# Kernel optimization log

Measured on AMD Instinct MI355X. Metric: run time of the kernel, lower is better.

The kernel has to match this reference:

```python
import jax, jax.numpy as jnp
import numpy as np
import math

B, CIN, COUT, NSC, H, W = 4, 3, 64, 3, 192, 192
HID = 64  # attention hidden channels


def setup_inputs() -> dict:
    key = jax.random.key(0)
    ks = jax.random.split(key, 10)
    pi = math.pi
    return {
        "x": jax.random.normal(ks[0], (B, CIN, H, W), jnp.float32),
        "freq": jax.random.uniform(ks[1], (NSC, COUT, CIN), jnp.float32) * pi,
        "theta": jax.random.uniform(ks[2], (NSC, COUT, CIN), jnp.float32) * pi,
        "sigma": jax.random.uniform(ks[3], (NSC, COUT, CIN), jnp.float32) * pi,
        "f0": jnp.ones((NSC, COUT, CIN), jnp.float32),
        "theta0": jnp.ones((NSC, COUT, CIN), jnp.float32),
        "attn_w1": jax.random.normal(ks[4], (HID, CIN), jnp.float32) / np.sqrt(CIN).astype(np.float32),
        "attn_b1": jnp.zeros((HID,), jnp.float32),
        "attn_w2": jax.random.normal(ks[5], (COUT * NSC, HID), jnp.float32) / np.sqrt(HID).astype(np.float32),
        "attn_b2": jnp.zeros((COUT * NSC,), jnp.float32),
        "bn_w": jnp.ones((COUT * NSC,), jnp.float32),
        "bn_b": jnp.zeros((COUT * NSC,), jnp.float32),
        "mixing_param": jax.random.uniform(ks[6], (1,), jnp.float32),
        "conv_w": jax.random.normal(ks[7], (COUT, CIN, 3, 3), jnp.float32) * 0.1,
        "freq_band_select": jax.random.uniform(ks[8], (COUT, CIN, 2), jnp.float32),
    }


def _forward(x, freq, theta, sigma, f0, theta0, attn_w1, attn_b1, attn_w2,
             attn_b2, bn_w, bn_b, mixing_param, conv_w, freq_band_select):
    b, cin, h, w = x.shape
    # torch.fft.fftshift default dim=None shifts ALL axes (incl. batch/channel)
    Xs = jnp.fft.fftshift(jnp.fft.fft2(x))  # [B,Cin,H,W] complex64

    # ---- multi-scale log-Gabor filter bank g[S,O,I,H,W] ----
    yy, xx = jnp.meshgrid(jnp.linspace(-1.0, 1.0, h), jnp.linspace(-1.0, 1.0, w), indexing="ij")
    r = jnp.sqrt(xx * xx + yy * yy + 1e-6)
    phi = jnp.arctan2(yy, xx)
    f0e = f0[..., None, None]
    sg = sigma[..., None, None]
    th = theta[..., None, None]
    th0 = theta0[..., None, None]
    fr = freq[..., None, None]
    log_gabor = jnp.exp(-(jnp.log(r) - jnp.log(f0e)) ** 2 / (2.0 * jnp.log(sg / f0e) ** 2))
    angular = jnp.exp(-(phi - th) ** 2 / (2.0 * th0 ** 2))
    g = log_gabor * angular * jnp.cos(fr * r) / (2.0 * math.pi * sg ** 2)  # [S,O,I,H,W]

    # ---- frequency attention: 1x1 conv -> ReLU -> 1x1 conv -> BN(train) -> softmax ----
    mag = jnp.abs(Xs)
    h1 = jax.nn.relu(jnp.einsum("oi,bihw->bohw", attn_w1, mag) + attn_b1[None, :, None, None])
    h2 = jnp.einsum("oi,bihw->bohw", attn_w2, h1) + attn_b2[None, :, None, None]
    mu = h2.mean(axis=(0, 2, 3))
    var = h2.var(axis=(0, 2, 3))  # biased, as torch BN training mode
    h2 = (h2 - mu[None, :, None, None]) * jax.lax.rsqrt(var + 1e-5)[None, :, None, None]
    h2 = h2 * bn_w[None, :, None, None] + bn_b[None, :, None, None]
    attn = jax.nn.softmax(h2, axis=1).reshape(b, NSC, COUT, h, w)  # view as [B,S,O,H,W]

    # ---- attention-weighted complex sum over (scale, out, in), then batch ----
    # attended_output(b) = sum_{s,o,i} attn[b,s,o]*g[s,o,i]*Xs[b,i]; torch then
    # sums over Cin and, via the [B,O,B,I,H,W] broadcast + sum(dims 2,3), over batch.
    Wr = jnp.einsum("bsohw,soihw->bihw", attn, g)  # real attention*filter weights
    A_tot = (Wr * Xs).sum(axis=(0, 1))             # [H,W] complex

    # ---- per-(out,in) frequency band mask (same index range on both axes) ----
    idx = jnp.floor((freq_band_select + 1.0) * 0.5 * h).astype(jnp.int32)  # [O,I,2]
    hr = jnp.arange(h)
    c = (hr[None, None, :] >= idx[..., 0:1]) & (hr[None, None, :] < idx[..., 1:2])  # [O,I,H]
    mask = (c[:, :, :, None] & c[:, :, None, :]).astype(jnp.float32)  # [O,I,H,W]
    Msum = mask.sum(axis=1)  # [O,H,W] (sum over Cin)

    # torch builds r[b0,o,b2,i,h,w]=A[b2]*M[o,i], ifftshift(all axes), ifft2,
    # real, sum over (b2,i). Rolls on summed axes commute with the sums, so this
    # equals ifftshift over (b0,o,h,w) of Q[b0,o]=A_tot*Msum[o] (const in b0).
    Q = jnp.broadcast_to((A_tot[None] * Msum.astype(Xs.dtype))[None], (b, COUT, h, w))
    xf = jnp.fft.ifft2(jnp.fft.ifftshift(Q)).real  # [B,O,H,W]

    xs = jax.lax.conv_general_dilated(
        x, conv_w, window_strides=(1, 1), padding=((1, 1), (1, 1)),
        dimension_numbers=("NCHW", "OIHW", "NCHW"))
    return mixing_param * xf + (1.0 - mixing_param) * xs


def reference(x, freq, theta, sigma, f0, theta0, attn_w1, attn_b1, attn_w2,
              attn_b2, bn_w, bn_b, mixing_param, conv_w, freq_band_select):
    return _forward(x, freq, theta, sigma, f0, theta0, attn_w1, attn_b1,
                    attn_w2, attn_b2, bn_w, bn_b, mixing_param, conv_w,
                    freq_band_select)
```

## Files before the change

kernel.cpp:

```cpp
#include <hip/hip_runtime.h>
#include <math.h>

#define NPIX  36864
#define PI2   6.28318530717958647692f

#define TW_OFF    0
#define PCA_OFF   1536
#define PCB_OFF   10752
#define W1F4_OFF  15360
#define W2B_OFF   16384
#define BN_OFF    65536
#define IDX_OFF   67072
#define M2_OFF    68608
#define T1_OFF    85248
#define XS_OFF    3624192
#define AH_OFF    7163136
#define XF_OFF    7458048
#define E2B_OFF   15846656
#define WS_FUSED  7458048
#define WS_SPLIT  16895232

#define PH_BYTES  14155776
#define E2C_OFF   14155776
#define OUT_MIN_ELEMS 9437184

typedef __attribute__((ext_vector_type(8))) short short8;
typedef __attribute__((ext_vector_type(4))) float floatx4;

__device__ __forceinline__ void bf16split(float v, unsigned short& hi, unsigned short& lo) {
    unsigned ub = __builtin_bit_cast(unsigned, v);
    hi = (unsigned short)(ub >> 16);
    float vh = __builtin_bit_cast(float, ub & 0xFFFF0000u);
    lo = (unsigned short)(__builtin_bit_cast(unsigned, v - vh) >> 16);
}

__global__ void k_pre(const float* freq, const float* theta, const float* sigma,
                      const float* f0, const float* theta0, const float* fbs,
                      const float* w1, const float* b1v, const float* w2,
                      char* ws, char* outw, int split) {
    float2* tw   = (float2*)(ws + TW_OFF);
    float4* pcA  = (float4*)(ws + PCA_OFF);
    float2* pcB  = (float2*)(ws + PCB_OFF);
    float4* w1f4 = (float4*)(ws + W1F4_OFF);
    unsigned short* w2b = (unsigned short*)(ws + W2B_OFF);
    int* idx = (int*)(ws + IDX_OFF);
    int gtid = blockIdx.x * blockDim.x + threadIdx.x;
    int gsz  = gridDim.x * blockDim.x;
    for (int n = gtid; n < 192; n += gsz) {
        float th = PI2 * (float)n / 192.0f;
        tw[n] = make_float2(cosf(th), sinf(th));
    }
    for (int t = gtid; t < 576; t += gsz) {
        int s = t / 192, rem = t % 192, o = rem / 3, i = rem % 3;
        float fr = freq[t], th = theta[t], sg = sigma[t], f0v = f0[t], th0 = theta0[t];
        float lg  = logf(sg / f0v);
        float a1  = -1.0f / (2.0f * lg * lg);
        float lf0 = logf(f0v);
        float a2  = -1.0f / (2.0f * th0 * th0);
        float lsc = -logf(PI2 * sg * sg);
        int pidx = (s*3 + i)*64 + o;
        pcA[pidx] = make_float4(a1, lf0, a2, th);
        pcB[pidx] = make_float2(fr, lsc);
    }
    for (int t = gtid; t < 64; t += gsz)
        w1f4[t] = make_float4(w1[t*3+0], w1[t*3+1], w1[t*3+2], b1v[t]);
    for (int u = gtid; u < 24576; u += gsz) {
        int j = u & 7;
        int l = (u >> 3) & 63;
        int hsel = (u >> 9) & 1;
        int rest = u >> 10;
        int kc = rest & 1;
        int t = rest >> 1;
        int k = kc*32 + (l>>4)*8 + j;
        int c = t*16 + (l & 15);
        float wv = w2[c*64 + k];
        unsigned short hi, lo;
        bf16split(wv, hi, lo);
        w2b[u] = hsel ? lo : hi;
    }
    for (int t = gtid; t < 192; t += gsz) {
        int lo = (int)floorf((fbs[t*2+0] + 1.0f) * 0.5f * 192.0f) - 96;
        int hi = (int)floorf((fbs[t*2+1] + 1.0f) * 0.5f * 192.0f) - 96;
        lo = max(0, min(96, lo));
        hi = max(0, min(96, hi));
        if (hi < lo) hi = lo;
        idx[t*2+0] = lo; idx[t*2+1] = hi;
    }
    if (split) {
        unsigned short* e2b = (unsigned short*)(ws + E2B_OFF);
        for (int u = gtid; u < 147456; u += gsz) {
            int j = u & 7;
            int l = (u >> 3) & 63;
            int half = (u >> 9) & 1;
            int rest = u >> 10;
            int kc = rest % 12, t = rest / 12;
            int k = kc*32 + ((l >> 4) << 3) + j;
            int w = k >> 1, comp = k & 1;
            int n = t*16 + (l & 15);
            int ang = (w * n) % 192;
            float th = PI2 * (float)ang / 192.0f;
            float v = comp ? sinf(th) : cosf(th);
            unsigned short hi, lo;
            bf16split(v, hi, lo);
            e2b[u] = half ? lo : hi;
        }
        unsigned short* e1 = (unsigned short*)(ws + T1_OFF);
        for (int u = gtid; u < 147456; u += gsz) {
            int j = u & 7;
            int l = (u >> 3) & 63;
            int half = (u >> 9) & 1;
            int rest = u >> 10;
            int kc = rest % 6;
            int comp = (rest / 6) & 1;
            int yt = rest / 12;
            int y = yt*16 + (l & 15);
            int h = kc*32 + ((l >> 4) << 3) + j;
            int ang = (h * y) % 192;
            float th = PI2 * (float)ang / 192.0f;
            float v = comp ? -sinf(th) : cosf(th);
            unsigned short hi, lo;
            bf16split(v, hi, lo);
            e1[u] = half ? lo : hi;
        }
        unsigned short* e2c = (unsigned short*)(outw + E2C_OFF);
        for (int u = gtid; u < 73728; u += gsz) {
            int j = u & 7;
            int l = (u >> 3) & 63;
            int half = (u >> 9) & 1;
            int rest = u >> 10;
            int kc = rest % 6, t = rest / 6;
            int k = kc*32 + ((l >> 4) << 3) + j;
            int w = k >> 1, comp = k & 1;
            int n = t*16 + (l & 15);
            int ang = (w * n) % 192;
            float th = PI2 * (float)ang / 192.0f;
            float v = comp ? sinf(th) : cosf(th);
            unsigned short hi, lo;
            bf16split(v, hi, lo);
            e2c[u] = half ? lo : hi;
        }
    }
}

__global__ __launch_bounds__(256) void k_dftm(const float* x, char* ws) {
    __shared__ __align__(16) float2 Ar[16][194];
    const unsigned short* e1  = (const unsigned short*)(ws + T1_OFF);
    const unsigned short* e2b = (const unsigned short*)(ws + E2B_OFF);
    float2* Xs = (float2*)(ws + XS_OFF);
    int tid = threadIdx.x;
    int bi = blockIdx.x / 12;
    int yt = blockIdx.x % 12;
    int y0 = yt * 16;
    int wave = tid >> 6, lane = tid & 63;
    int ml = lane & 15, qd = lane >> 4;
    const float* xp = x + bi * NPIX;
    union AB { short8 v; unsigned short u[8]; };
    floatx4 s1re[3], s1im[3];
#pragma unroll
    for (int tt = 0; tt < 3; tt++) {
        s1re[tt] = (floatx4){0.f,0.f,0.f,0.f};
        s1im[tt] = (floatx4){0.f,0.f,0.f,0.f};
    }
#pragma unroll 1
    for (int kc = 0; kc < 6; kc++) {
        const unsigned short* ac = e1 + (((((yt*2 + 0)*6 + kc)*2) << 9) + (lane << 3));
        const unsigned short* as = e1 + (((((yt*2 + 1)*6 + kc)*2) << 9) + (lane << 3));
        short8 ach = *(const short8*)ac;
        short8 acl = *(const short8*)(ac + 512);
        short8 ash = *(const short8*)as;
        short8 asl = *(const short8*)(as + 512);
#pragma unroll
        for (int tt = 0; tt < 3; tt++) {
            int nt = wave*3 + tt;
            AB bh8, bl8;
#pragma unroll
            for (int j = 0; j < 8; j++) {
                int h = kc*32 + qd*8 + j;
                float xv = xp[h*192 + nt*16 + ml];
                bf16split(xv, bh8.u[j], bl8.u[j]);
            }
            floatx4 r = s1re[tt];
            r = __builtin_amdgcn_mfma_f32_16x16x32_bf16(ach, bh8.v, r, 0, 0, 0);
            r = __builtin_amdgcn_mfma_f32_16x16x32_bf16(acl, bh8.v, r, 0, 0, 0);
            r = __builtin_amdgcn_mfma_f32_16x16x32_bf16(ach, bl8.v, r, 0, 0, 0);
            s1re[tt] = r;
            floatx4 q = s1im[tt];
            q = __builtin_amdgcn_mfma_f32_16x16x32_bf16(ash, bh8.v, q, 0, 0, 0);
            q = __builtin_amdgcn_mfma_f32_16x16x32_bf16(asl, bh8.v, q, 0, 0, 0);
            q = __builtin_amdgcn_mfma_f32_16x16x32_bf16(ash, bl8.v, q, 0, 0, 0);
            s1im[tt] = q;
        }
    }
#pragma unroll
    for (int tt = 0; tt < 3; tt++) {
        int w = (wave*3 + tt)*16 + ml;
#pragma unroll
        for (int r = 0; r < 4; r++)
            Ar[qd*4 + r][w] = make_float2(s1re[tt][r], s1im[tt][r]);
    }
    __syncthreads();
    floatx4 accre[3], accim[3];
#pragma unroll
    for (int tt = 0; tt < 3; tt++) {
        accre[tt] = (floatx4){0.f,0.f,0.f,0.f};
        accim[tt] = (floatx4){0.f,0.f,0.f,0.f};
    }
#pragma unroll 1
    for (int kc = 0; kc < 12; kc++) {
        int wb = kc*16 + qd*4;
        float4 p01 = *(const float4*)&Ar[ml][wb];
        float4 p23 = *(const float4*)&Ar[ml][wb + 2];
        float av[8]  = {p01.x, p01.y, p01.z, p01.w, p23.x, p23.y, p23.z, p23.w};
        float apv[8] = {p01.y, -p01.x, p01.w, -p01.z, p23.y, -p23.x, p23.w, -p23.z};
        AB ah, al, aph, apl;
#pragma unroll
        for (int j = 0; j < 8; j++) {
            bf16split(av[j],  ah.u[j],  al.u[j]);
            bf16split(apv[j], aph.u[j], apl.u[j]);
        }
#pragma unroll
        for (int tt = 0; tt < 3; tt++) {
            int t = wave*3 + tt;
            const unsigned short* bp = e2b + (((t*12 + kc)*2) << 9) + (lane << 3);
            short8 bh = *(const short8*)bp;
            short8 bl = *(const short8*)(bp + 512);
            floatx4 r = accre[tt];
            r = __builtin_amdgcn_mfma_f32_16x16x32_bf16(ah.v,  bh, r, 0, 0, 0);
            r = __builtin_amdgcn_mfma_f32_16x16x32_bf16(al.v,  bh, r, 0, 0, 0);
            r = __builtin_amdgcn_mfma_f32_16x16x32_bf16(ah.v,  bl, r, 0, 0, 0);
            accre[tt] = r;
            floatx4 q = accim[tt];
            q = __builtin_amdgcn_mfma_f32_16x16x32_bf16(aph.v, bh, q, 0, 0, 0);
            q = __builtin_amdgcn_mfma_f32_16x16x32_bf16(apl.v, bh, q, 0, 0, 0);
            q = __builtin_amdgcn_mfma_f32_16x16x32_bf16(aph.v, bl, q, 0, 0, 0);
            accim[tt] = q;
        }
    }
    int b = bi / 3, i = bi % 3;
    int bs = (b + 2) & 3;
    int is = (i + 1) % 3;
    float2* Xp = Xs + (bs*3 + is)*NPIX;
#pragma unroll
    for (int tt = 0; tt < 3; tt++) {
        int kx = (wave*3 + tt)*16 + ml;
        int ks = kx + 96; if (ks >= 192) ks -= 192;
#pragma unroll
        for (int r = 0; r < 4; r++) {
            int y = y0 + qd*4 + r;
            int ys = y + 96; if (ys >= 192) ys -= 192;
            Xp[ys*192 + ks] = make_float2(accre[tt][r], accim[tt][r]);
        }
    }
}

__global__ __launch_bounds__(192) void k_dft1(const float* x, char* ws) {
    __shared__ float2 twsh[192];
    const float2* tw = (const float2*)(ws + TW_OFF);
    float2* t1 = (float2*)(ws + T1_OFF);
    int tid = threadIdx.x;
    twsh[tid] = tw[tid];
    __syncthreads();
    int bi = blockIdx.x;
    int y0 = blockIdx.y * 4;
    int w  = tid;
    const float* xp = x + bi * NPIX;
    float2 acc[4];
#pragma unroll
    for (int d = 0; d < 4; d++) acc[d] = make_float2(0.f, 0.f);
    for (int h = 0; h < 192; h++) {
        float xv = xp[h*192 + w];
        int m = (h * y0) % 192;
#pragma unroll
        for (int d = 0; d < 4; d++) {
            float2 e = twsh[m];
            acc[d].x += xv * e.x;
            acc[d].y -= xv * e.y;
            m += h; if (m >= 192) m -= 192;
        }
    }
    float2* op = t1 + bi * NPIX;
#pragma unroll
    for (int d = 0; d < 4; d++) op[(y0 + d)*192 + w] = acc[d];
}

__global__ __launch_bounds__(192) void k_dft2(char* ws) {
    __shared__ float2 twsh[192];
    __shared__ float2 row[192];
    const float2* tw = (const float2*)(ws + TW_OFF);
    const float2* t1a = (const float2*)(ws + T1_OFF);
    float2* Xs = (float2*)(ws + XS_OFF);
    int tid = threadIdx.x;
    int bi = blockIdx.x, y = blockIdx.y;
    twsh[tid] = tw[tid];
    row[tid] = t1a[bi*NPIX + y*192 + tid];
    __syncthreads();
    int kx = tid;
    float2 st = twsh[kx];
    float2 acc = make_float2(0.f, 0.f);
#pragma unroll 1
    for (int w0 = 0; w0 < 192; w0 += 32) {
        float2 e = twsh[(w0 * kx) % 192];
#pragma unroll
        for (int w = 0; w < 32; w++) {
            float2 t = row[w0 + w];
            acc.x += t.x*e.x + t.y*e.y;
            acc.y += t.y*e.x - t.x*e.y;
            float ex = e.x*st.x - e.y*st.y;
            e.y = e.x*st.y + e.y*st.x;
            e.x = ex;
        }
    }
    int b = bi / 3, i = bi % 3;
    int bs = (b + 2) & 3;
    int is = (i + 1) % 3;
    int ys = y + 96;  if (ys >= 192) ys -= 192;
    int ks = kx + 96; if (ks >= 192) ks -= 192;
    Xs[(bs*3 + is)*NPIX + ys*192 + ks] = acc;
}

__global__ __launch_bounds__(256) void k_stats(char* ws) {
    __shared__ float magL[192];
    __shared__ float4 w1L[64];
    __shared__ float m1L[64];
    __shared__ __align__(16) unsigned short fragH[512*8];
    __shared__ __align__(16) unsigned short fragL[512*8];
    const float2* Xs = (const float2*)(ws + XS_OFF);
    float* M2 = (float*)(ws + M2_OFF);
    int tid = threadIdx.x;
    int wave = tid >> 6, lane = tid & 63;
    if (tid < 64) { w1L[tid] = ((const float4*)(ws + W1F4_OFF))[tid]; m1L[tid] = 0.f; }
    __syncthreads();
    int cch = wave*16 + (lane & 15);
    float4 wf = w1L[cch];
    float msum = 0.f;
    floatx4 acc[4];
#pragma unroll
    for (int nb = 0; nb < 4; nb++) acc[nb] = (floatx4){0.f, 0.f, 0.f, 0.f};
    union AB { short8 v; unsigned short u[8]; };
#pragma unroll 1
    for (int it = 0; it < 2; it++) {
        int tile = blockIdx.x * 2 + it;
        int S0 = tile * 64;
        int b = S0 / NPIX;
        int p0 = S0 - b*NPIX;
        if (tid < 192) {
            int i = tid >> 6, s = tid & 63;
            float2 v = Xs[(b*3 + i)*NPIX + p0 + s];
            magL[s*3 + i] = sqrtf(v.x*v.x + v.y*v.y);
        }
        __syncthreads();
#pragma unroll
        for (int kc = 0; kc < 2; kc++) {
            AB h8, l8;
#pragma unroll
            for (int j = 0; j < 8; j++) {
                int s = kc*32 + (lane>>4)*8 + j;
                float mg0 = magL[s*3], mg1 = magL[s*3+1], mg2 = magL[s*3+2];
                float hv = fmaxf(wf.w + wf.x*mg0 + wf.y*mg1 + wf.z*mg2, 0.f);
                msum += hv;
                bf16split(hv, h8.u[j], l8.u[j]);
            }
            int z = (kc*4 + wave)*64 + lane;
            *(short8*)&fragH[z*8] = h8.v;
            *(short8*)&fragL[z*8] = l8.v;
        }
        __syncthreads();
        short8 Ah0 = *(const short8*)&fragH[((0*4+wave)*64 + lane)*8];
        short8 Ah1 = *(const short8*)&fragH[((1*4+wave)*64 + lane)*8];
        short8 Al0 = *(const short8*)&fragL[((0*4+wave)*64 + lane)*8];
        short8 Al1 = *(const short8*)&fragL[((1*4+wave)*64 + lane)*8];
#pragma unroll
        for (int nb = 0; nb < 4; nb++) {
            short8 Bh0 = *(const short8*)&fragH[((0*4+nb)*64 + lane)*8];
            short8 Bh1 = *(const short8*)&fragH[((1*4+nb)*64 + lane)*8];
            short8 Bl0 = *(const short8*)&fragL[((0*4+nb)*64 + lane)*8];
            short8 Bl1 = *(const short8*)&fragL[((1*4+nb)*64 + lane)*8];
            floatx4 a = acc[nb];
            a = __builtin_amdgcn_mfma_f32_16x16x32_bf16(Ah0, Bh0, a, 0, 0, 0);
            a = __builtin_amdgcn_mfma_f32_16x16x32_bf16(Al0, Bh0, a, 0, 0, 0);
            a = __builtin_amdgcn_mfma_f32_16x16x32_bf16(Ah0, Bl0, a, 0, 0, 0);
            a = __builtin_amdgcn_mfma_f32_16x16x32_bf16(Ah1, Bh1, a, 0, 0, 0);
            a = __builtin_amdgcn_mfma_f32_16x16x32_bf16(Al1, Bh1, a, 0, 0, 0);
            a = __builtin_amdgcn_mfma_f32_16x16x32_bf16(Ah1, Bl1, a, 0, 0, 0);
            acc[nb] = a;
        }
        __syncthreads();
    }
#pragma unroll
    for (int nb = 0; nb < 4; nb++)
#pragma unroll
        for (int r = 0; r < 4; r++) {
            int row = wave*16 + (lane>>4)*4 + r;
            int col = nb*16 + (lane & 15);
            atomicAdd(&M2[row*64 + col], acc[nb][r]);
        }
    atomicAdd(&m1L[cch], msum);
    __syncthreads();
    if (tid < 64) atomicAdd(&M2[4096 + tid], m1L[tid]);
}

__global__ __launch_bounds__(64) void k_bn(const float* w2, const float* bnw,
                                           const float* bnb, char* ws) {
    const float* M2 = (const float*)(ws + M2_OFF);
    const float* m1 = M2 + 4096;
    float* bnsc = (float*)(ws + BN_OFF);
    float* bnsh = bnsc + 192;
    int c = blockIdx.x;
    int jj = threadIdx.x;
    const float* row = w2 + c*64;
    float rj = row[jj];
    float inner = 0.f;
    const float* m2r = M2 + jj*64;
    for (int k = 0; k < 64; k++) inner += row[k] * m2r[k];
    float qpart = rj * inner;
    float dpart = rj * m1[jj];
#pragma unroll
    for (int sh = 32; sh >= 1; sh >>= 1) {
        qpart += __shfl_xor(qpart, sh);
        dpart += __shfl_xor(dpart, sh);
    }
    if (jj == 0) {
        const float invN = 1.0f / 147456.0f;
        float d = dpart * invN;
        float qv = qpart * invN;
        float var = qv - d*d;
        float rstd = rsqrtf(var + 1e-5f);
        float scale = bnw[c] * rstd;
        bnsc[c] = scale;
        bnsh[c] = bnb[c] - d * scale;
    }
}

__global__ __launch_bounds__(256) void k_attn(char* ws) {
    __shared__ __align__(16) float4 pcAL[576];
    __shared__ float2 pcBL[576];
    __shared__ float4 w1L[64];
    const float2* Xs = (const float2*)(ws + XS_OFF);
    const float* bnA = (const float*)(ws + BN_OFF);
    const char* W2G = (const char*)(ws + W2B_OFF);
    float2* Ah = (float2*)(ws + AH_OFF);
    int tid = threadIdx.x;
    {
        const float4* pcA4 = (const float4*)(ws + PCA_OFF);
        const float2* pcB2 = (const float2*)(ws + PCB_OFF);
        for (int u = tid; u < 576; u += 256) {
            pcAL[u] = pcA4[u];
            pcBL[u] = pcB2[u];
        }
        if (tid < 64) w1L[tid] = ((const float4*)(ws + W1F4_OFF))[tid];
    }
    __syncthreads();
    int wave = tid >> 6, lane = tid & 63;
    int cl = lane & 15, q = lane >> 4;
    int g = blockIdx.x * 4 + wave;
    int pix0 = g * 4;

    union AB { short8 v; unsigned short u[8]; };
    int pb = pix0 + (cl >> 2), bb = cl & 3;
    float2 q0 = Xs[(bb*3+0)*NPIX + pb];
    float2 q1 = Xs[(bb*3+1)*NPIX + pb];
    float2 q2 = Xs[(bb*3+2)*NPIX + pb];
    float mg0 = sqrtf(q0.x*q0.x + q0.y*q0.y);
    float mg1 = sqrtf(q1.x*q1.x + q1.y*q1.y);
    float mg2 = sqrtf(q2.x*q2.x + q2.y*q2.y);
    AB ah[2], al[2];
#pragma unroll
    for (int kc = 0; kc < 2; kc++)
#pragma unroll
        for (int j = 0; j < 8; j++) {
            int k = kc*32 + q*8 + j;
            float4 wf = w1L[k];
            float hv = fmaxf(wf.w + wf.x*mg0 + wf.y*mg1 + wf.z*mg2, 0.f);
            bf16split(hv, ah[kc].u[j], al[kc].u[j]);
        }
    int pixE = pix0 + q;
    int hh = pixE / 192, ww = pixE - hh*192;
    float yy = -1.0f + (float)hh * (2.0f/191.0f);
    float xx = -1.0f + (float)ww * (2.0f/191.0f);
    float rr = sqrtf(xx*xx + yy*yy + 1e-6f);
    float lr = __logf(rr);
    float phi = atan2f(yy, xx);
    float sm0 = 0.f, sm1 = 0.f, sm2 = 0.f, sm3 = 0.f;
    float Wr[4][3];
#pragma unroll
    for (int r = 0; r < 4; r++) { Wr[r][0] = 0.f; Wr[r][1] = 0.f; Wr[r][2] = 0.f; }
#pragma unroll 2
    for (int t = 0; t < 12; t++) {
        floatx4 a = {0.f, 0.f, 0.f, 0.f};
#pragma unroll
        for (int kc = 0; kc < 2; kc++) {
            int ob = (((t*2 + kc)*2)*64 + lane)*16;
            short8 bh = *(const short8*)(W2G + ob);
            short8 bl = *(const short8*)(W2G + ob + 1024);
            a = __builtin_amdgcn_mfma_f32_16x16x32_bf16(ah[kc].v, bh, a, 0, 0, 0);
            a = __builtin_amdgcn_mfma_f32_16x16x32_bf16(al[kc].v, bh, a, 0, 0, 0);
            a = __builtin_amdgcn_mfma_f32_16x16x32_bf16(ah[kc].v, bl, a, 0, 0, 0);
        }
        int c = t*16 + cl;
        float sc_ = bnA[c], sh_ = bnA[192 + c];
        float e0 = __expf(a[0]*sc_ + sh_);
        float e1 = __expf(a[1]*sc_ + sh_);
        float e2 = __expf(a[2]*sc_ + sh_);
        float e3 = __expf(a[3]*sc_ + sh_);
        sm0 += e0; sm1 += e1; sm2 += e2; sm3 += e3;
        int sB = c >> 6, o = c & 63;
#pragma unroll
        for (int i = 0; i < 3; i++) {
            int pidx = (sB*3 + i)*64 + o;
            float4 pa = pcAL[pidx];
            float2 pbv = pcBL[pidx];
            float dl = lr - pa.y, dp = phi - pa.w;
            float gv = __expf(pa.x*dl*dl + pa.z*dp*dp + pbv.y) * __cosf(pbv.x*rr);
            Wr[0][i] += e0*gv; Wr[1][i] += e1*gv;
            Wr[2][i] += e2*gv; Wr[3][i] += e3*gv;
        }
    }
#pragma unroll
    for (int sh = 1; sh < 16; sh <<= 1) {
        sm0 += __shfl_xor(sm0, sh); sm1 += __shfl_xor(sm1, sh);
        sm2 += __shfl_xor(sm2, sh); sm3 += __shfl_xor(sm3, sh);
    }
    float inv0 = 1.0f/sm0, inv1 = 1.0f/sm1, inv2 = 1.0f/sm2, inv3 = 1.0f/sm3;
    float are = 0.f, aim = 0.f;
#pragma unroll
    for (int i = 0; i < 3; i++) {
        float2 x0 = Xs[(0*3+i)*NPIX + pixE];
        float2 x1 = Xs[(1*3+i)*NPIX + pixE];
        float2 x2 = Xs[(2*3+i)*NPIX + pixE];
        float2 x3 = Xs[(3*3+i)*NPIX + pixE];
        float w0v = Wr[0][i]*inv0, w1v = Wr[1][i]*inv1;
        float w2v = Wr[2][i]*inv2, w3v = Wr[3][i]*inv3;
        are += w0v*x0.x + w1v*x1.x + w2v*x2.x + w3v*x3.x;
        aim += w0v*x0.y + w1v*x1.y + w2v*x2.y + w3v*x3.y;
    }
#pragma unroll
    for (int sh = 1; sh < 16; sh <<= 1) {
        are += __shfl_xor(are, sh);
        aim += __shfl_xor(aim, sh);
    }
    if (cl == 0) {
        int hs = hh + 96; if (hs >= 192) hs -= 192;
        int wsx = ww + 96; if (wsx >= 192) wsx -= 192;
        Ah[hs*192 + wsx] = make_float2(are, aim);
    }
}

__global__ __launch_bounds__(64) void k_phpre(char* ws, char* outw) {
    __shared__ float2 AhL[96];
    const float2* tw  = (const float2*)(ws + TW_OFF);
    const float2* Ahp = (const float2*)(ws + AH_OFF);
    float2* Ph = (float2*)outw;
    int tid = threadIdx.x;
    int y = blockIdx.y * 64 + tid;
    int w = blockIdx.x;
    for (int u = tid; u < 96; u += 64) AhL[u] = Ahp[u*192 + w];
    __syncthreads();
    float2 step = tw[y];
    float ex = 1.f, ey = 0.f;
    float ax = 0.f, ay = 0.f;
    for (int h = 0; h < 96; h++) {
        float2 a = AhL[h];
        ax += a.x*ex - a.y*ey;
        ay += a.x*ey + a.y*ex;
        Ph[(h*96 + w)*192 + y] = make_float2(ax, ay);
        float t = ex*step.x - ey*step.y;
        ey = ex*step.y + ey*step.x;
        ex = t;
    }
}

__global__ __launch_bounds__(256) void k_ifftm(char* ws, char* outw) {
    __shared__ __align__(16) unsigned short AhiL[16*200];
    __shared__ __align__(16) unsigned short AloL[16*200];
    __shared__ int iL[3], iH[3];
    const float2* Ph = (const float2*)outw;
    const unsigned short* e2c = (const unsigned short*)(outw + E2C_OFF);
    const int* idx = (const int*)(ws + IDX_OFF);
    float* xf = (float*)(ws + XF_OFF);
    int tid = threadIdx.x;
    int o  = blockIdx.x / 12;
    int ys = blockIdx.x % 12;
    int op = (o + 32) & 63;
    if (tid < 3) { iL[tid] = idx[(op*3 + tid)*2]; iH[tid] = idx[(op*3 + tid)*2 + 1]; }
    __syncthreads();
    for (int u = tid; u < 1536; u += 256) {
        int w = u >> 4, yy = u & 15;
        int y = ys*16 + yy;
        float sr = 0.f, si = 0.f;
#pragma unroll
        for (int i = 0; i < 3; i++) {
            int lo = iL[i], hi = iH[i];
            if (w >= lo && w < hi) {
                float2 a = Ph[((hi-1)*96 + w)*192 + y];
                sr += a.x; si += a.y;
                if (lo > 0) {
                    float2 b2 = Ph[((lo-1)*96 + w)*192 + y];
                    sr -= b2.x; si -= b2.y;
                }
            }
        }
        unsigned short rh, rl, ih, il;
        bf16split(sr, rh, rl);
        bf16split(-si, ih, il);
        *(unsigned*)&AhiL[yy*200 + 2*w] = (unsigned)rh | ((unsigned)ih << 16);
        *(unsigned*)&AloL[yy*200 + 2*w] = (unsigned)rl | ((unsigned)il << 16);
    }
    __syncthreads();
    int wave = tid >> 6, lane = tid & 63;
    int ml = lane & 15, qd = lane >> 4;
    const float s = 1.0f / 36864.0f;
#pragma unroll 1
    for (int ntl = 0; ntl < 3; ntl++) {
        int nt = wave*3 + ntl;
        floatx4 acc = (floatx4){0.f,0.f,0.f,0.f};
#pragma unroll
        for (int kc = 0; kc < 6; kc++) {
            const unsigned short* bp = e2c + ((nt*6 + kc) << 10) + (lane << 3);
            short8 bh = *(const short8*)bp;
            short8 bl = *(const short8*)(bp + 512);
            int ka = kc*32 + qd*8;
            short8 ah = *(const short8*)&AhiL[ml*200 + ka];
            short8 al = *(const short8*)&AloL[ml*200 + ka];
            acc = __builtin_amdgcn_mfma_f32_16x16x32_bf16(ah, bh, acc, 0, 0, 0);
            acc = __builtin_amdgcn_mfma_f32_16x16x32_bf16(al, bh, acc, 0, 0, 0);
            acc = __builtin_amdgcn_mfma_f32_16x16x32_bf16(ah, bl, acc, 0, 0, 0);
        }
#pragma unroll
        for (int r = 0; r < 4; r++) {
            int y = ys*16 + qd*4 + r;
            int x = nt*16 + ml;
            xf[o*NPIX + y*192 + x] = acc[r] * s;
        }
    }
}

__global__ __launch_bounds__(192) void k_conv(const float* x, const float* convw,
                                              const float* mixp, const float* xf,
                                              float* out) {
    int col = threadIdx.x;
    int y = blockIdx.x;
    int b = blockIdx.y;
    int o0 = blockIdx.z * 16;
    float xv[27];
#pragma unroll
    for (int i = 0; i < 3; i++)
#pragma unroll
        for (int dy = 0; dy < 3; dy++)
#pragma unroll
            for (int dx = 0; dx < 3; dx++) {
                int yq = y + dy - 1, xq = col + dx - 1;
                bool ok = (yq >= 0) & (yq < 192) & (xq >= 0) & (xq < 192);
                xv[(i*3 + dy)*3 + dx] = ok ? x[(b*3+i)*NPIX + yq*192 + xq] : 0.f;
            }
    float mixv = mixp[0];
    float onem = 1.0f - mixv;
    for (int o = o0; o < o0 + 16; o++) {
        float s = 0.f;
#pragma unroll
        for (int c = 0; c < 27; c++) s += xv[c] * convw[o*27 + c];
        float xfv = xf[o*NPIX + y*192 + col];
        out[((b*64 + o)*192 + y)*192 + col] = mixv*xfv + onem*s;
    }
}

__global__ __launch_bounds__(192) void k_final(const float* x, const float* convw,
                                               const float* mixp, float* out, char* ws) {
    __shared__ float2 twsh[192];
    __shared__ float2 Ssh[3][96];
    __shared__ float cwsh[27];
    __shared__ int iL[3], iH[3];
    const float2* tw = (const float2*)(ws + TW_OFF);
    const int* idx = (const int*)(ws + IDX_OFF);
    const float2* Ah = (const float2*)(ws + AH_OFF);
    int tid = threadIdx.x;
    int y = blockIdx.x;
    int o = blockIdx.y;
    int op = (o + 32) & 63;
    twsh[tid] = tw[tid];
    if (tid < 27) cwsh[tid] = convw[o*27 + tid];
    if (tid < 3) { iL[tid] = idx[(op*3 + tid)*2]; iH[tid] = idx[(op*3 + tid)*2 + 1]; }
    __syncthreads();
    int l0 = iL[0], u0 = iH[0], l1 = iL[1], u1 = iH[1], l2 = iL[2], u2 = iH[2];
    int n0 = u0 - l0, n1 = u1 - l1, n2 = u2 - l2;
    int p1 = n0 + n1, T = p1 + n2;
    for (int t = tid; t < T; t += 192) {
        int i, off, lo, hi;
        if (t < n0)      { i = 0; off = t;      lo = l0; hi = u0; }
        else if (t < p1) { i = 1; off = t - n0; lo = l1; hi = u1; }
        else             { i = 2; off = t - p1; lo = l2; hi = u2; }
        int wq = lo + off;
        float sx = 0.f, sy = 0.f;
        int m = (lo * y) % 192;
        for (int hq = lo; hq < hi; hq++) {
            float2 a = Ah[hq*192 + wq];
            float2 e = twsh[m];
            sx += a.x*e.x - a.y*e.y;
            sy += a.x*e.y + a.y*e.x;
            m += y; if (m >= 192) m -= 192;
        }
        Ssh[i][off] = make_float2(sx, sy);
    }
    __syncthreads();
    int col = tid;
    float accre = 0.f;
#pragma unroll
    for (int i = 0; i < 3; i++) {
        int lo = iL[i];
        int wi = iH[i] - lo;
        int m = (lo * col) % 192;
        for (int off = 0; off < wi; off++) {
            float2 S = Ssh[i][off];
            float2 e = twsh[m];
            accre += S.x*e.x - S.y*e.y;
            m += col; if (m >= 192) m -= 192;
        }
    }
    float xfv = accre * (1.0f / 36864.0f);
    float mixv = mixp[0];
    float onem = 1.0f - mixv;
#pragma unroll
    for (int b = 0; b < 4; b++) {
        float s = 0.f;
#pragma unroll
        for (int i = 0; i < 3; i++) {
            const float* xp = x + (b*3 + i)*NPIX;
#pragma unroll
            for (int dy = -1; dy <= 1; dy++) {
                int yq = y + dy;
                if (yq < 0 || yq >= 192) continue;
                const float* rowp = xp + yq*192;
#pragma unroll
                for (int dx = -1; dx <= 1; dx++) {
                    int xq = col + dx;
                    if (xq < 0 || xq >= 192) continue;
                    s += rowp[xq] * cwsh[i*9 + (dy+1)*3 + (dx+1)];
                }
            }
        }
        out[((b*64 + o)*192 + y)*192 + col] = mixv*xfv + onem*s;
    }
}

extern "C" void kernel_launch(void* const* d_in, const int* in_sizes, int n_in,
                              void* d_out, int out_size, void* d_ws, size_t ws_size,
                              hipStream_t stream) {
    const float* x      = (const float*)d_in[0];
    const float* freq   = (const float*)d_in[1];
    const float* theta  = (const float*)d_in[2];
    const float* sigma  = (const float*)d_in[3];
    const float* f0     = (const float*)d_in[4];
    const float* theta0 = (const float*)d_in[5];
    const float* aw1    = (const float*)d_in[6];
    const float* ab1    = (const float*)d_in[7];
    const float* aw2    = (const float*)d_in[8];
    const float* bnw    = (const float*)d_in[10];
    const float* bnb    = (const float*)d_in[11];
    const float* mixp   = (const float*)d_in[12];
    const float* convw  = (const float*)d_in[13];
    const float* fbs    = (const float*)d_in[14];
    float* out = (float*)d_out;
    char* ws = (char*)d_ws;
    char* outc = (char*)d_out;
    if (ws_size < (size_t)WS_FUSED) return;
    int split = (ws_size >= (size_t)WS_SPLIT) && (out_size >= OUT_MIN_ELEMS);

    hipMemsetAsync(ws + M2_OFF, 0, 16640, stream);
    k_pre  <<<192, 256, 0, stream>>>(freq, theta, sigma, f0, theta0, fbs,
                                     aw1, ab1, aw2, ws, outc, split);
    if (split) {
        k_dftm <<<144, 256, 0, stream>>>(x, ws);
    } else {
        k_dft1 <<<dim3(12, 48), 192, 0, stream>>>(x, ws);
        k_dft2 <<<dim3(12, 192), 192, 0, stream>>>(ws);
    }
    k_stats<<<1152, 256, 0, stream>>>(ws);
    k_bn   <<<192, 64, 0, stream>>>(aw2, bnw, bnb, ws);
    k_attn <<<2304, 256, 0, stream>>>(ws);
    if (split) {
        k_phpre<<<dim3(96, 3), 64, 0, stream>>>(ws, outc);
        k_ifftm<<<768, 256, 0, stream>>>(ws, outc);
        k_conv <<<dim3(192, 4, 4), 192, 0, stream>>>(x, convw, mixp,
                                                     (const float*)(ws + XF_OFF), out);
    } else {
        k_final<<<dim3(192, 64), 192, 0, stream>>>(x, convw, mixp, out, ws);
    }
}
```

Measured before the change: 241.3 us.

## Fuse inverse-DFT matmul with conv/mix epilogue and move prefix buffers into workspace

The 3x3 convolution and mixing step is now computed inside the MFMA inverse-DFT kernel's epilogue, and the final output is written there for all four batches. This removes the intermediate xf buffer round trip and one kernel launch. The prefix-sum Ph table and the e2c twiddles move from the output buffer into split regions of the workspace, since the output can no longer serve as scratch. In exchange, the epilogue reads x with scattered, uncoalesced loads and redoes the conv taps per (o, batch) with an unroll-1 loop, which may add latency.

```diff
diff --git a/kernel.cpp b/kernel.cpp
--- a/kernel.cpp
+++ b/kernel.cpp
@@ -20,9 +20,9 @@
 #define WS_FUSED  7458048
 #define WS_SPLIT  16895232
 
-#define PH_BYTES  14155776
-#define E2C_OFF   14155776
-#define OUT_MIN_ELEMS 9437184
+#define PHA_OFF   380160
+#define PHB_OFF   7458048
+#define E2C2_OFF  16141568
 
 typedef __attribute__((ext_vector_type(8))) short short8;
 typedef __attribute__((ext_vector_type(4))) float floatx4;
@@ -37,7 +37,7 @@
 __global__ void k_pre(const float* freq, const float* theta, const float* sigma,
                       const float* f0, const float* theta0, const float* fbs,
                       const float* w1, const float* b1v, const float* w2,
-                      char* ws, char* outw, int split) {
+                      char* ws, int split) {
     float2* tw   = (float2*)(ws + TW_OFF);
     float4* pcA  = (float4*)(ws + PCA_OFF);
     float2* pcB  = (float2*)(ws + PCB_OFF);
@@ -122,7 +122,7 @@
             bf16split(v, hi, lo);
             e1[u] = half ? lo : hi;
         }
-        unsigned short* e2c = (unsigned short*)(outw + E2C_OFF);
+        unsigned short* e2c = (unsigned short*)(ws + E2C2_OFF);
         for (int u = gtid; u < 73728; u += gsz) {
             int j = u & 7;
             int l = (u >> 3) & 63;
@@ -545,11 +545,12 @@
     }
 }
 
-__global__ __launch_bounds__(64) void k_phpre(char* ws, char* outw) {
+__global__ __launch_bounds__(64) void k_phpre(char* ws) {
     __shared__ float2 AhL[96];
     const float2* tw  = (const float2*)(ws + TW_OFF);
     const float2* Ahp = (const float2*)(ws + AH_OFF);
-    float2* Ph = (float2*)outw;
+    float2* PhA = (float2*)(ws + PHA_OFF);
+    float2* PhB = (float2*)(ws + PHB_OFF);
     int tid = threadIdx.x;
     int y = blockIdx.y * 64 + tid;
     int w = blockIdx.x;
@@ -562,21 +563,26 @@
         float2 a = AhL[h];
         ax += a.x*ex - a.y*ey;
         ay += a.x*ey + a.y*ex;
-        Ph[(h*96 + w)*192 + y] = make_float2(ax, ay);
+        float2* dst = (h < 46) ? (PhA + ((size_t)(h*96 + w))*192)
+                               : (PhB + ((size_t)((h-46)*96 + w))*192);
+        dst[y] = make_float2(ax, ay);
         float t = ex*step.x - ey*step.y;
         ey = ex*step.y + ey*step.x;
         ex = t;
     }
 }
 
-__global__ __launch_bounds__(256) void k_ifftm(char* ws, char* outw) {
+__global__ __launch_bounds__(256) void k_ifc(char* ws, const float* __restrict__ x,
+                                             const float* __restrict__ convw,
+                                             const float* __restrict__ mixp,
+                                             float* __restrict__ out) {
     __shared__ __align__(16) unsigned short AhiL[16*200];
     __shared__ __align__(16) unsigned short AloL[16*200];
     __shared__ int iL[3], iH[3];
-    const float2* Ph = (const float2*)outw;
-    const unsigned short* e2c = (const unsigned short*)(outw + E2C_OFF);
+    const float2* PhA = (const float2*)(ws + PHA_OFF);
+    const float2* PhB = (const float2*)(ws + PHB_OFF);
+    const unsigned short* e2c = (const unsigned short*)(ws + E2C2_OFF);
     const int* idx = (const int*)(ws + IDX_OFF);
-    float* xf = (float*)(ws + XF_OFF);
     int tid = threadIdx.x;
     int o  = blockIdx.x / 12;
     int ys = blockIdx.x % 12;
@@ -591,10 +597,14 @@
         for (int i = 0; i < 3; i++) {
             int lo = iL[i], hi = iH[i];
             if (w >= lo && w < hi) {
-                float2 a = Ph[((hi-1)*96 + w)*192 + y];
+                int lv = hi - 1;
+                float2 a = (lv < 46) ? PhA[((size_t)(lv*96 + w))*192 + y]
+                                     : PhB[((size_t)((lv-46)*96 + w))*192 + y];
                 sr += a.x; si += a.y;
                 if (lo > 0) {
-                    float2 b2 = Ph[((lo-1)*96 + w)*192 + y];
+                    int lv2 = lo - 1;
+                    float2 b2 = (lv2 < 46) ? PhA[((size_t)(lv2*96 + w))*192 + y]
+                                           : PhB[((size_t)((lv2-46)*96 + w))*192 + y];
                     sr -= b2.x; si -= b2.y;
                 }
             }
@@ -606,6 +616,11 @@
         *(unsigned*)&AloL[yy*200 + 2*w] = (unsigned)rl | ((unsigned)il << 16);
     }
     __syncthreads();
+    float cw[27];
+#pragma unroll
+    for (int c = 0; c < 27; c++) cw[c] = convw[o*27 + c];
+    float mixv = mixp[0];
+    float onem = 1.0f - mixv;
     int wave = tid >> 6, lane = tid & 63;
     int ml = lane & 15, qd = lane >> 4;
     const float s = 1.0f / 36864.0f;
@@ -625,41 +640,28 @@
             acc = __builtin_amdgcn_mfma_f32_16x16x32_bf16(al, bh, acc, 0, 0, 0);
             acc = __builtin_amdgcn_mfma_f32_16x16x32_bf16(ah, bl, acc, 0, 0, 0);
         }
-#pragma unroll
+        int xcol = nt*16 + ml;
+#pragma unroll 1
         for (int r = 0; r < 4; r++) {
             int y = ys*16 + qd*4 + r;
-            int x = nt*16 + ml;
-            xf[o*NPIX + y*192 + x] = acc[r] * s;
-        }
-    }
-}
-
-__global__ __launch_bounds__(192) void k_conv(const float* x, const float* convw,
-                                              const float* mixp, const float* xf,
-                                              float* out) {
-    int col = threadIdx.x;
-    int y = blockIdx.x;
-    int b = blockIdx.y;
-    int o0 = blockIdx.z * 16;
-    float xv[27];
-#pragma unroll
-    for (int i = 0; i < 3; i++)
-#pragma unroll
-        for (int dy = 0; dy < 3; dy++)
-#pragma unroll
-            for (int dx = 0; dx < 3; dx++) {
-                int yq = y + dy - 1, xq = col + dx - 1;
-                bool ok = (yq >= 0) & (yq < 192) & (xq >= 0) & (xq < 192);
-                xv[(i*3 + dy)*3 + dx] = ok ? x[(b*3+i)*NPIX + yq*192 + xq] : 0.f;
+            float xfv = acc[r] * s;
+#pragma unroll
+            for (int b = 0; b < 4; b++) {
+                float s2 = 0.f;
+#pragma unroll
+                for (int i = 0; i < 3; i++)
+#pragma unroll
+                    for (int dy = 0; dy < 3; dy++)
+#pragma unroll
+                        for (int dx = 0; dx < 3; dx++) {
+                            int yq = y + dy - 1, xq = xcol + dx - 1;
+                            bool ok = (yq >= 0) & (yq < 192) & (xq >= 0) & (xq < 192);
+                            float xvv = ok ? x[(b*3+i)*NPIX + yq*192 + xq] : 0.f;
+                            s2 += xvv * cw[(i*3 + dy)*3 + dx];
+                        }
+                out[((b*64 + o)*192 + y)*192 + xcol] = mixv*xfv + onem*s2;
             }
-    float mixv = mixp[0];
-    float onem = 1.0f - mixv;
-    for (int o = o0; o < o0 + 16; o++) {
-        float s = 0.f;
-#pragma unroll
-        for (int c = 0; c < 27; c++) s += xv[c] * convw[o*27 + c];
-        float xfv = xf[o*NPIX + y*192 + col];
-        out[((b*64 + o)*192 + y)*192 + col] = mixv*xfv + onem*s;
+        }
     }
 }
 
@@ -760,13 +762,12 @@
     const float* fbs    = (const float*)d_in[14];
     float* out = (float*)d_out;
     char* ws = (char*)d_ws;
-    char* outc = (char*)d_out;
     if (ws_size < (size_t)WS_FUSED) return;
-    int split = (ws_size >= (size_t)WS_SPLIT) && (out_size >= OUT_MIN_ELEMS);
+    int split = (ws_size >= (size_t)WS_SPLIT);
 
     hipMemsetAsync(ws + M2_OFF, 0, 16640, stream);
     k_pre  <<<192, 256, 0, stream>>>(freq, theta, sigma, f0, theta0, fbs,
-                                     aw1, ab1, aw2, ws, outc, split);
+                                     aw1, ab1, aw2, ws, split);
     if (split) {
         k_dftm <<<144, 256, 0, stream>>>(x, ws);
     } else {
@@ -777,10 +778,8 @@
     k_bn   <<<192, 64, 0, stream>>>(aw2, bnw, bnb, ws);
     k_attn <<<2304, 256, 0, stream>>>(ws);
     if (split) {
-        k_phpre<<<dim3(96, 3), 64, 0, stream>>>(ws, outc);
-        k_ifftm<<<768, 256, 0, stream>>>(ws, outc);
-        k_conv <<<dim3(192, 4, 4), 192, 0, stream>>>(x, convw, mixp,
-                                                     (const float*)(ws + XF_OFF), out);
+        k_phpre<<<dim3(96, 3), 64, 0, stream>>>(ws);
+        k_ifc  <<<768, 256, 0, stream>>>(ws, x, convw, mixp, out);
     } else {
         k_final<<<dim3(192, 64), 192, 0, stream>>>(x, convw, mixp, out, ws);
     }
```

Result: slower. 249.0 us (+3.2%).
